# Optimization experiments

Measured on AMD Instinct MI355X. Metric: run time of the kernel, lower is better.

## Reference

```python
import jax, jax.numpy as jnp
import numpy as np

ALPHA = 0.3  # LeakyReLU negative slope
NEG_INF = -1e9


def setup_inputs() -> dict:
    key = jax.random.key(0)
    k1, k2, k3, k4 = jax.random.split(key, 4)
    B, N, C_IN, C_OUT, H = 4, 2048, 128, 128, 4
    node_feats = jax.random.normal(k1, (B, N, C_IN), dtype=jnp.float32)
    # xavier_uniform with gain 1.414 for projection weight [c_out, c_in]
    limit_w = 1.414 * np.sqrt(6.0 / (C_IN + C_OUT))
    W = jax.random.uniform(k2, (C_OUT, C_IN), minval=-limit_w, maxval=limit_w, dtype=jnp.float32)
    b = jnp.zeros((C_OUT,), dtype=jnp.float32)
    c_head = C_OUT // H
    limit_a = 1.414 * np.sqrt(6.0 / (H + 2 * c_head))
    a = jax.random.uniform(k3, (H, 2 * c_head), minval=-limit_a, maxval=limit_a, dtype=jnp.float32)
    return {"node_feats": node_feats, "W": W, "b": b, "a": a}


def reference(node_feats, W, b, a):
    B, N, _ = node_feats.shape
    H, two_c = a.shape
    c = two_c // 2
    # dynamic adjacency: cosine similarity, sigmoid > 0.5  <=>  sim > 0
    nf = node_feats / jnp.maximum(jnp.linalg.norm(node_feats, axis=-1, keepdims=True), 1e-12)
    sim = jnp.einsum('bid,bjd->bij', nf, nf)            # [B,N,N]
    mask = sim > 0.0                                     # adjacency (sigmoid(sim) > 0.5)
    # projection -> per-head features [B,N,H,c]
    h = (node_feats @ W.T + b).reshape(B, N, H, c)
    # edge score a . [h_i, h_j] decomposes into left/right parts
    a_l, a_r = a[:, :c], a[:, c:]                        # [H,c] each
    s_l = jnp.einsum('bnhc,hc->bnh', h, a_l)             # [B,N,H]
    s_r = jnp.einsum('bnhc,hc->bnh', h, a_r)             # [B,N,H]
    logits = jax.nn.leaky_relu(s_l[:, :, None, :] + s_r[:, None, :, :], ALPHA)  # [B,N,N,H]
    attn = jnp.where(mask[..., None], logits, NEG_INF)
    probs = jax.nn.softmax(attn, axis=2)                 # softmax over source nodes j
    # dropout is identity in eval mode
    out = jnp.einsum('bijh,bjhc->bihc', probs, h)
    return out.reshape(B, N, -1)                         # concat heads
```

## Files before the change

kernel.cpp:

```cpp
#include <hip/hip_runtime.h>
#include <cstdint>
#include <cstddef>

typedef float v16f __attribute__((ext_vector_type(16)));
typedef short v8s  __attribute__((ext_vector_type(8)));

#define MFMA32(A,B,C) __builtin_amdgcn_mfma_f32_32x32x16_bf16((A),(B),(C),0,0,0)
#define THRU 1e-3f
#define SEG 16

__device__ __forceinline__ unsigned f2bf(float f) {
  unsigned u = __builtin_bit_cast(unsigned, f);
  u += 0x7FFFu + ((u >> 16) & 1u);
  return u >> 16;
}
__device__ __forceinline__ float bf2f(unsigned us) {
  return __builtin_bit_cast(float, us << 16);
}
__device__ __forceinline__ void gload16(const void* g, void* l) {
  __builtin_amdgcn_global_load_lds(
      (const __attribute__((address_space(1))) void*)g,
      (__attribute__((address_space(3))) void*)l, 16, 0, 0);
}

__global__ __launch_bounds__(256) void gat_prep(
    const float* __restrict__ nf, const float* __restrict__ Wm,
    const float* __restrict__ bias, const float* __restrict__ aw,
    unsigned short* __restrict__ nfh, unsigned short* __restrict__ nfm,
    unsigned short* __restrict__ ht,
    float* __restrict__ EFl, float* __restrict__ EFrp)
{
  __shared__ float xl[32][132];
  const int tid = threadIdx.x;
  const int row = tid & 31, g = tid >> 5;
  const int r0 = blockIdx.x * 32;
  const int b = r0 >> 11, n0 = r0 & 2047;
  const int d0 = g * 16;

  float x[16];
  {
    const float* xp = nf + (size_t)(r0 + row) * 128 + d0;
#pragma unroll
    for (int q = 0; q < 4; ++q) {
      float4 v = *(const float4*)(xp + 4 * q);
      x[4*q+0] = v.x; x[4*q+1] = v.y; x[4*q+2] = v.z; x[4*q+3] = v.w;
    }
  }
  {
    unsigned hu[16], mu[16];
#pragma unroll
    for (int q = 0; q < 16; ++q) {
      xl[row][d0 + q] = x[q];
      unsigned hb = f2bf(x[q]); float hf = bf2f(hb);
      unsigned mb = f2bf(x[q] - hf);
      hu[q] = hb; mu[q] = mb;
    }
    const size_t to = ((size_t)(b * 64 + (n0 >> 5)) * 8 + g) * 512 + row * 8;
    uint4 p0, p1;
    p0.x = hu[0] | (hu[1] << 16);  p0.y = hu[2] | (hu[3] << 16);
    p0.z = hu[4] | (hu[5] << 16);  p0.w = hu[6] | (hu[7] << 16);
    p1.x = hu[8] | (hu[9] << 16);  p1.y = hu[10] | (hu[11] << 16);
    p1.z = hu[12] | (hu[13] << 16); p1.w = hu[14] | (hu[15] << 16);
    *(uint4*)(nfh + to) = p0; *(uint4*)(nfh + to + 256) = p1;
    p0.x = mu[0] | (mu[1] << 16);  p0.y = mu[2] | (mu[3] << 16);
    p0.z = mu[4] | (mu[5] << 16);  p0.w = mu[6] | (mu[7] << 16);
    p1.x = mu[8] | (mu[9] << 16);  p1.y = mu[10] | (mu[11] << 16);
    p1.z = mu[12] | (mu[13] << 16); p1.w = mu[14] | (mu[15] << 16);
    *(uint4*)(nfm + to) = p0; *(uint4*)(nfm + to + 256) = p1;
  }
  __syncthreads();

  float acc[16];
  const int ob = g * 16;
#pragma unroll
  for (int o = 0; o < 16; ++o) acc[o] = bias[ob + o];
  for (int dd = 0; dd < 128; dd += 4) {
    float4 xq = *(const float4*)&xl[row][dd];
#pragma unroll
    for (int o = 0; o < 16; ++o) {
      float4 wq = *(const float4*)(Wm + (size_t)(ob + o) * 128 + dd);
      acc[o] = fmaf(xq.x, wq.x, acc[o]);
      acc[o] = fmaf(xq.y, wq.y, acc[o]);
      acc[o] = fmaf(xq.z, wq.z, acc[o]);
      acc[o] = fmaf(xq.w, wq.w, acc[o]);
    }
  }
#pragma unroll
  for (int o = 0; o < 16; ++o)
    ht[((size_t)b * 128 + ob + o) * 2048 + n0 + row] = (unsigned short)f2bf(acc[o]);

  const int hh = g >> 1, cb = (g & 1) * 16;
  float sl = 0.f, sr = 0.f;
#pragma unroll
  for (int o = 0; o < 16; ++o) {
    sl = fmaf(acc[o], aw[hh * 64 + cb + o], sl);
    sr = fmaf(acc[o], aw[hh * 64 + 32 + cb + o], sr);
  }
  sl += __shfl_xor(sl, 32, 64);
  sr += __shfl_xor(sr, 32, 64);
  if (!(g & 1)) {
    const float L2E = 1.4426950408889634f;
    float El = exp2f(sl * L2E), Fl = exp2f(sl * (0.3f * L2E));
    float Er = exp2f(sr * L2E), Fr = exp2f(sr * (0.3f * L2E));
    size_t nn = (size_t)(r0 + row);
    EFl[nn * 8 + hh]     = El;
    EFl[nn * 8 + 4 + hh] = Fl;
    EFrp[nn * 8 + (hh >> 1) * 4 + (hh & 1) * 2]     = Er;
    EFrp[nn * 8 + (hh >> 1) * 4 + (hh & 1) * 2 + 1] = Fr;
  }
}

__global__ __launch_bounds__(256) void gat_mask(
    const unsigned short* __restrict__ nfh, const unsigned short* __restrict__ nfm,
    unsigned* __restrict__ mask, unsigned* __restrict__ list,
    unsigned* __restrict__ lcnt)
{
  const int tid = threadIdx.x, lane = tid & 63, wv = tid >> 6;
  const int li = lane & 31, hi = lane >> 5;
  const int blk = blockIdx.x;
  const int jb = blk & 31, t = blk >> 5;
  const int ib = t & 15, b = t >> 4;
  const int i0 = ib * 128 + wv * 32;
  const int j0 = jb * 64;
  const int wid = blk * 4 + wv;

  const size_t lbyte = (size_t)lane * 8;
  const size_t tiB  = ((size_t)(b * 64 + (i0 >> 5)) * 8) * 512 + lbyte;
  const size_t tjA0 = ((size_t)(b * 64 + (j0 >> 5)) * 8) * 512 + lbyte;
  const size_t tjA1 = tjA0 + 4096;

  v8s BH[8], BM[8];
#pragma unroll
  for (int kc = 0; kc < 8; ++kc) {
    BH[kc] = *(const v8s*)(nfh + tiB + kc * 512);
    BM[kc] = *(const v8s*)(nfm + tiB + kc * 512);
  }

  v16f S0, S1;
#pragma unroll
  for (int r = 0; r < 16; ++r) { S0[r] = 0.f; S1[r] = 0.f; }
#pragma unroll
  for (int kc = 0; kc < 8; ++kc) {
    v8s A0h = *(const v8s*)(nfh + tjA0 + kc * 512);
    v8s A1h = *(const v8s*)(nfh + tjA1 + kc * 512);
    v8s A0m = *(const v8s*)(nfm + tjA0 + kc * 512);
    v8s A1m = *(const v8s*)(nfm + tjA1 + kc * 512);
    S0 = MFMA32(A0h, BH[kc], S0);
    S1 = MFMA32(A1h, BH[kc], S1);
    S0 = MFMA32(A0h, BM[kc], S0);
    S1 = MFMA32(A1h, BM[kc], S1);
    S0 = MFMA32(A0m, BH[kc], S0);
    S1 = MFMA32(A1m, BH[kc], S1);
  }

  unsigned u0 = 0, u1 = 0;
  float mn = 1e30f;
  const int sh = hi * 4;
#pragma unroll
  for (int r = 0; r < 16; ++r) {
    const int jlc = (r & 3) + 8 * (r >> 2);
    const unsigned bit = (1u << jlc) << sh;
    if (S0[r] > 0.f) u0 |= bit;
    if (S1[r] > 0.f) u1 |= bit;
    mn = fminf(mn, fabsf(S0[r]));
    mn = fminf(mn, fabsf(S1[r]));
  }
  {
    unsigned f0 = u0 | (unsigned)__shfl_xor((int)u0, 32, 64);
    unsigned f1 = u1 | (unsigned)__shfl_xor((int)u1, 32, 64);
    if (hi == 0) {
      mask[(size_t)(b * 64 + jb * 2)     * 2048 + i0 + li] = f0;
      mask[(size_t)(b * 64 + jb * 2 + 1) * 2048 + i0 + li] = f1;
    }
  }

  int wcount = 0;
  if (__ballot(mn < THRU)) {
#pragma unroll
    for (int sub = 0; sub < 2; ++sub) {
#pragma unroll
      for (int r = 0; r < 16; ++r) {
        const int jl = (r & 3) + 8 * (r >> 2) + 4 * hi;
        const float s = sub ? S1[r] : S0[r];
        const bool f = fabsf(s) < THRU;
        unsigned long long bal = __ballot(f);
        if (bal) {
          if (f) {
            int pos = wcount + (int)__popcll(bal & ((1ull << lane) - 1ull));
            if (pos < SEG)
              list[wid * SEG + pos] =
                  (unsigned)((b << 22) | ((i0 + li) << 11) | (j0 + sub * 32 + jl));
          }
          wcount += (int)__popcll(bal);
        }
      }
    }
    if (wcount > SEG) wcount = SEG;
  }
  if (lane == 0) lcnt[wid] = (unsigned)wcount;
}

__global__ __launch_bounds__(256) void gat_fix(
    const float* __restrict__ nf, const unsigned* __restrict__ list,
    const unsigned* __restrict__ lcnt, unsigned* __restrict__ mask)
{
  const unsigned t = blockIdx.x * 256 + threadIdx.x;
  const unsigned seg = t >> 4, slot = t & (SEG - 1);
  if (slot >= lcnt[seg]) return;
  const unsigned e = list[t];
  const int b = e >> 22, i = (e >> 11) & 2047, j = e & 2047;
  const float* xi = nf + ((size_t)b * 2048 + i) * 128;
  const float* xj = nf + ((size_t)b * 2048 + j) * 128;
  double acc = 0.0;
#pragma unroll 8
  for (int k = 0; k < 128; k += 4) {
    float4 a = *(const float4*)(xi + k);
    float4 c = *(const float4*)(xj + k);
    acc = fma((double)a.x, (double)c.x, acc);
    acc = fma((double)a.y, (double)c.y, acc);
    acc = fma((double)a.z, (double)c.z, acc);
    acc = fma((double)a.w, (double)c.w, acc);
  }
  unsigned* w = &mask[(size_t)(b * 64 + (j >> 5)) * 2048 + i];
  const unsigned bit = 1u << (j & 31);
  if (acc > 0.0) atomicOr(w, bit); else atomicAnd(w, ~bit);
}

#define PVBLK(pw, h)                                                           \
  {                                                                            \
    auto q0 = __builtin_amdgcn_permlane32_swap((int)pw[0], (int)pw[2], false, false); \
    auto q1 = __builtin_amdgcn_permlane32_swap((int)pw[1], (int)pw[3], false, false); \
    auto q2 = __builtin_amdgcn_permlane32_swap((int)pw[4], (int)pw[6], false, false); \
    auto q3 = __builtin_amdgcn_permlane32_swap((int)pw[5], (int)pw[7], false, false); \
    uint4 c0, c1;                                                              \
    c0.x = (unsigned)q0[0]; c0.y = (unsigned)q1[0];                            \
    c0.z = (unsigned)q0[1]; c0.w = (unsigned)q1[1];                            \
    c1.x = (unsigned)q2[0]; c1.y = (unsigned)q3[0];                            \
    c1.z = (unsigned)q2[1]; c1.w = (unsigned)q3[1];                            \
    v8s P0 = __builtin_bit_cast(v8s, c0);                                      \
    v8s P1 = __builtin_bit_cast(v8s, c1);                                      \
    const int cc = (h) * 32 + li;                                              \
    const char* vr = sm + cc * 256;                                            \
    const int cx = cc & 15;                                                    \
    v8s V0 = *(const v8s*)(vr + ((((it2 << 2) + hi) ^ cx) << 4));              \
    v8s V1 = *(const v8s*)(vr + ((((it2 << 2) + 2 + hi) ^ cx) << 4));          \
    acc[h] = MFMA32(P0, V0, acc[h]);                                           \
    acc[h] = MFMA32(P1, V1, acc[h]);                                           \
  }

__global__ __launch_bounds__(256, 2) void gat_attn(
    const unsigned short* __restrict__ ht, const float* __restrict__ EFl,
    const float* __restrict__ EFrp, const unsigned* __restrict__ mask,
    float* __restrict__ nump, float* __restrict__ denp, const int CH)
{
  __shared__ __align__(16) char sm[16384 + 2048];
  const int JPC = 2048 / CH, H = JPC >> 7;
  const int tid = threadIdx.x, lane = tid & 63, wv = tid >> 6;
  const int li = lane & 31, hi = lane >> 5;

  const int blk = blockIdx.x;
  const int x = blk & 7, y = blk >> 3;
  const int ig = y & 15;
  const int combo = x * CH + (y >> 4);
  const int hp2 = combo & 1;
  const int r2 = combo >> 1;
  const int ch = r2 % CH, b = r2 / CH;

  const size_t nb = (size_t)b * 2048;
  const int i0 = ig * 128 + wv * 32;
  const int j0 = ch * JPC;

  float EL[2], FL[2];
  {
    const float* p = EFl + (nb + i0 + li) * 8 + 2 * hp2;
    float2 e = *(const float2*)p;
    float2 f = *(const float2*)(p + 4);
    EL[0] = e.x; EL[1] = e.y; FL[0] = f.x; FL[1] = f.y;
  }

  v16f acc[2];
#pragma unroll
  for (int h = 0; h < 2; ++h)
#pragma unroll
    for (int r = 0; r < 16; ++r) acc[h][r] = 0.f;
  float den[2] = {0.f, 0.f};

  for (int h0 = 0; h0 < H; ++h0) {
    if (h0) __syncthreads();
    const int jbase = j0 + (h0 << 7);
    {
      const size_t cbase = (size_t)b * 128 + (hp2 << 6);
#pragma unroll
      for (int s = 0; s < 4; ++s) {
        const int L = s * 4096 + tid * 16;
        const int c = L >> 8, gs = (L >> 4) & 15;
        const int g = gs ^ (c & 15);
        gload16((const char*)ht + (((cbase + c) * 2048 + jbase) << 1) + (g << 4),
                sm + L);
      }
      if (tid < 128)
        gload16((const char*)EFrp + (size_t)(nb + jbase + tid) * 32 + (hp2 << 4),
                sm + 16384 + tid * 16);
    }
    unsigned mw[4];
#pragma unroll
    for (int q = 0; q < 4; ++q)
      mw[q] = mask[(size_t)(b * 64 + (jbase >> 5) + q) * 2048 + i0 + li] >> (hi * 4);
    __syncthreads();

#pragma unroll
    for (int it2 = 0; it2 < 4; ++it2) {
      const char* Eb = sm + 16384 + (it2 << 9);
      const unsigned mh = mw[it2];
      unsigned pA[8], pB[8];
#pragma unroll
      for (int rp = 0; rp < 8; ++rp) {
        const int r0 = 2 * rp;
        const int jl0c = (r0 & 3) + 8 * (r0 >> 2);
        const int nA = (jl0c + 4 * hi) * 16;
        float4 e0 = *(const float4*)(Eb + nA);
        float4 e1 = *(const float4*)(Eb + nA + 16);
        const bool m0 = (mh >> jl0c) & 1;
        const bool m1 = (mh >> (jl0c + 1)) & 1;
        float wA0 = fmaxf(e0.x * EL[0], e0.y * FL[0]); wA0 = m0 ? wA0 : 0.f;
        float wB0 = fmaxf(e0.z * EL[1], e0.w * FL[1]); wB0 = m0 ? wB0 : 0.f;
        float wA1 = fmaxf(e1.x * EL[0], e1.y * FL[0]); wA1 = m1 ? wA1 : 0.f;
        float wB1 = fmaxf(e1.z * EL[1], e1.w * FL[1]); wB1 = m1 ? wB1 : 0.f;
        den[0] += wA0 + wA1;
        den[1] += wB0 + wB1;
        asm("v_cvt_pk_bf16_f32 %0, %1, %2" : "=v"(pA[rp]) : "v"(wA0), "v"(wA1));
        asm("v_cvt_pk_bf16_f32 %0, %1, %2" : "=v"(pB[rp]) : "v"(wB0), "v"(wB1));
      }
      PVBLK(pA, 0)
      PVBLK(pB, 1)
    }
  }

#pragma unroll
  for (int h = 0; h < 2; ++h) den[h] += __shfl_xor(den[h], 32, 64);

  const size_t obase = ((size_t)b * CH + ch) * 2048 + i0;
#pragma unroll
  for (int h = 0; h < 2; ++h) {
#pragma unroll
    for (int r = 0; r < 16; ++r) {
      const int il = (r & 3) + 8 * (r >> 2) + 4 * hi;
      nump[(obase + il) * 128 + (hp2 * 2 + h) * 32 + li] = acc[h][r];
    }
  }
  if (lane < 32) {
    float2 dv; dv.x = den[0]; dv.y = den[1];
    *(float2*)(denp + (obase + li) * 4 + 2 * hp2) = dv;
  }
}

__global__ __launch_bounds__(256) void gat_reduce(
    const float* __restrict__ nump, const float* __restrict__ denp,
    float* __restrict__ out, const int CH)
{
  const int idx = blockIdx.x * 256 + threadIdx.x;
  const int b = idx >> 18;
  const int rem = idx & 262143;
  const int n = rem >> 7;
  const int col = rem & 127;
  const int h = col >> 5;
  float s = 0.f, d = 0.f;
  for (int ch = 0; ch < CH; ++ch) {
    s += nump[(((size_t)b * CH + ch) * 2048 + n) * 128 + col];
    d += denp[(((size_t)b * CH + ch) * 2048 + n) * 4 + h];
  }
  out[idx] = s / d;
}

extern "C" void kernel_launch(void* const* d_in, const int* in_sizes, int n_in,
                              void* d_out, int out_size, void* d_ws, size_t ws_size,
                              hipStream_t stream) {
  const float* nf   = (const float*)d_in[0];
  const float* Wm   = (const float*)d_in[1];
  const float* bias = (const float*)d_in[2];
  const float* aw   = (const float*)d_in[3];
  float* out = (float*)d_out;
  char* ws = (char*)d_ws;

  unsigned short* nfh  = (unsigned short*)(ws);
  unsigned short* nfm  = (unsigned short*)(ws + 2097152);
  unsigned short* ht   = (unsigned short*)(ws + 4194304);
  float*    EFl  = (float*)(ws + 6291456);
  float*    EFrp = (float*)(ws + 6553600);
  unsigned* mask = (unsigned*)(ws + 6815744);
  unsigned* list = (unsigned*)(ws + 8912896);
  unsigned* lcnt = (unsigned*)(ws + 9437184);
  const size_t o_den = 9469952;

  int CH = 8;
  if (ws_size < o_den + 8ull * 4325376ull) CH = 4;

  float* denp = (float*)(ws + o_den);
  float* nump = (float*)(ws + o_den + (size_t)CH * 131072);

  gat_prep<<<256, 256, 0, stream>>>(nf, Wm, bias, aw, nfh, nfm, ht, EFl, EFrp);
  gat_mask<<<2048, 256, 0, stream>>>(nfh, nfm, mask, list, lcnt);
  gat_fix<<<512, 256, 0, stream>>>(nf, list, lcnt, mask);
  gat_attn<<<128 * CH, 256, 0, stream>>>(ht, EFl, EFrp, mask, nump, denp, CH);
  gat_reduce<<<4096, 256, 0, stream>>>(nump, denp, out, CH);
}
```

Baseline: 75.02 us.

## Double-buffer LDS staging in attention kernel and hoist mask loads

Turns the attention kernel's per-chunk LDS staging of V and right-edge factors into a two-buffer ping-pong. The next chunk's async global-to-LDS loads are issued before computing on the current one, so memory latency overlaps with the MFMA work. All mask words for the block's j-range are loaded once up front, and CH becomes a template parameter so loop trip counts are compile-time constants. LDS use doubles to about 36KB per block and register pressure rises. With CH=8 there are only two chunks per block, which limits how much overlap is possible.

```diff
diff --git a/kernel.cpp b/kernel.cpp
--- a/kernel.cpp
+++ b/kernel.cpp
@@ -226,7 +226,7 @@
   if (acc > 0.0) atomicOr(w, bit); else atomicAnd(w, ~bit);
 }
 
-#define PVBLK(pw, h)                                                           \
+#define PVBLK(pw, h, smv)                                                      \
   {                                                                            \
     auto q0 = __builtin_amdgcn_permlane32_swap((int)pw[0], (int)pw[2], false, false); \
     auto q1 = __builtin_amdgcn_permlane32_swap((int)pw[1], (int)pw[3], false, false); \
@@ -240,7 +240,7 @@
     v8s P0 = __builtin_bit_cast(v8s, c0);                                      \
     v8s P1 = __builtin_bit_cast(v8s, c1);                                      \
     const int cc = (h) * 32 + li;                                              \
-    const char* vr = sm + cc * 256;                                            \
+    const char* vr = (smv) + cc * 256;                                         \
     const int cx = cc & 15;                                                    \
     v8s V0 = *(const v8s*)(vr + ((((it2 << 2) + hi) ^ cx) << 4));              \
     v8s V1 = *(const v8s*)(vr + ((((it2 << 2) + 2 + hi) ^ cx) << 4));          \
@@ -248,13 +248,17 @@
     acc[h] = MFMA32(P1, V1, acc[h]);                                           \
   }
 
+template<int CH>
 __global__ __launch_bounds__(256, 2) void gat_attn(
     const unsigned short* __restrict__ ht, const float* __restrict__ EFl,
     const float* __restrict__ EFrp, const unsigned* __restrict__ mask,
-    float* __restrict__ nump, float* __restrict__ denp, const int CH)
+    float* __restrict__ nump, float* __restrict__ denp)
 {
-  __shared__ __align__(16) char sm[16384 + 2048];
-  const int JPC = 2048 / CH, H = JPC >> 7;
+  constexpr int JPC = 2048 / CH;
+  constexpr int H = JPC >> 7;
+  constexpr int MW = JPC >> 5;
+  __shared__ __align__(16) char sm[2][18432];
+
   const int tid = threadIdx.x, lane = tid & 63, wv = tid >> 6;
   const int li = lane & 31, hi = lane >> 5;
 
@@ -278,6 +282,11 @@
     EL[0] = e.x; EL[1] = e.y; FL[0] = f.x; FL[1] = f.y;
   }
 
+  unsigned mw[MW];
+#pragma unroll
+  for (int q = 0; q < MW; ++q)
+    mw[q] = mask[(size_t)(b * 64 + (j0 >> 5) + q) * 2048 + i0 + li] >> (hi * 4);
+
   v16f acc[2];
 #pragma unroll
   for (int h = 0; h < 2; ++h)
@@ -285,33 +294,35 @@
     for (int r = 0; r < 16; ++r) acc[h][r] = 0.f;
   float den[2] = {0.f, 0.f};
 
+  auto STAGE = [&](int h0, int p) {
+    const int jbase = j0 + (h0 << 7);
+    const size_t cbase = (size_t)b * 128 + (hp2 << 6);
+#pragma unroll
+    for (int s = 0; s < 4; ++s) {
+      const int L = s * 4096 + tid * 16;
+      const int c = L >> 8, gs = (L >> 4) & 15;
+      const int g = gs ^ (c & 15);
+      gload16((const char*)ht + (((cbase + c) * 2048 + jbase) << 1) + (g << 4),
+              sm[p] + L);
+    }
+    if (tid < 128)
+      gload16((const char*)EFrp + (size_t)(nb + jbase + tid) * 32 + (hp2 << 4),
+              sm[p] + 16384 + tid * 16);
+  };
+
+  STAGE(0, 0);
+  __syncthreads();
+
+#pragma unroll
   for (int h0 = 0; h0 < H; ++h0) {
+    const int p = h0 & 1;
     if (h0) __syncthreads();
-    const int jbase = j0 + (h0 << 7);
-    {
-      const size_t cbase = (size_t)b * 128 + (hp2 << 6);
-#pragma unroll
-      for (int s = 0; s < 4; ++s) {
-        const int L = s * 4096 + tid * 16;
-        const int c = L >> 8, gs = (L >> 4) & 15;
-        const int g = gs ^ (c & 15);
-        gload16((const char*)ht + (((cbase + c) * 2048 + jbase) << 1) + (g << 4),
-                sm + L);
-      }
-      if (tid < 128)
-        gload16((const char*)EFrp + (size_t)(nb + jbase + tid) * 32 + (hp2 << 4),
-                sm + 16384 + tid * 16);
-    }
-    unsigned mw[4];
-#pragma unroll
-    for (int q = 0; q < 4; ++q)
-      mw[q] = mask[(size_t)(b * 64 + (jbase >> 5) + q) * 2048 + i0 + li] >> (hi * 4);
-    __syncthreads();
+    if (h0 + 1 < H) STAGE(h0 + 1, p ^ 1);
 
 #pragma unroll
     for (int it2 = 0; it2 < 4; ++it2) {
-      const char* Eb = sm + 16384 + (it2 << 9);
-      const unsigned mh = mw[it2];
+      const char* Eb = sm[p] + 16384 + (it2 << 9);
+      const unsigned mh = mw[(h0 << 2) + it2];
       unsigned pA[8], pB[8];
 #pragma unroll
       for (int rp = 0; rp < 8; ++rp) {
@@ -331,8 +342,8 @@
         asm("v_cvt_pk_bf16_f32 %0, %1, %2" : "=v"(pA[rp]) : "v"(wA0), "v"(wA1));
         asm("v_cvt_pk_bf16_f32 %0, %1, %2" : "=v"(pB[rp]) : "v"(wB0), "v"(wB1));
       }
-      PVBLK(pA, 0)
-      PVBLK(pB, 1)
+      PVBLK(pA, 0, sm[p])
+      PVBLK(pB, 1, sm[p])
     }
   }
 
@@ -401,6 +412,9 @@
   gat_prep<<<256, 256, 0, stream>>>(nf, Wm, bias, aw, nfh, nfm, ht, EFl, EFrp);
   gat_mask<<<2048, 256, 0, stream>>>(nfh, nfm, mask, list, lcnt);
   gat_fix<<<512, 256, 0, stream>>>(nf, list, lcnt, mask);
-  gat_attn<<<128 * CH, 256, 0, stream>>>(ht, EFl, EFrp, mask, nump, denp, CH);
+  if (CH == 8)
+    gat_attn<8><<<1024, 256, 0, stream>>>(ht, EFl, EFrp, mask, nump, denp);
+  else
+    gat_attn<4><<<512, 256, 0, stream>>>(ht, EFl, EFrp, mask, nump, denp);
   gat_reduce<<<4096, 256, 0, stream>>>(nump, denp, out, CH);
 }
```

New measurement: 74.88 us. No clear change (-0.2%).
